# Kernel tuning notes

Measured on AMD Instinct MI355X. Metric: run time of the kernel, lower is better.

Reference implementation:

```python
import jax, jax.numpy as jnp
import numpy as np

B, NNODES, E, IN, H, FEAS = 32, 1024, 262144, 8, 128, 64


def setup_inputs() -> dict:
    key = jax.random.key(0)
    ks = jax.random.split(key, 24)
    N = B * NNODES
    s = 0.05
    x = jax.random.normal(ks[0], (N, IN), jnp.float32)
    edge_index = jax.random.randint(ks[1], (2, E), 0, N)
    batch_vec = jnp.repeat(jnp.arange(B), NNODES)
    rows_local = jax.random.randint(ks[2], (B, FEAS), 0, NNODES)
    mask_rows = (rows_local + jnp.arange(B)[:, None] * NNODES).reshape(-1)
    mask_cols = jax.random.randint(ks[3], (B * FEAS,), 0, NNODES)
    inp = dict(x=x, edge_index=edge_index, batch_vec=batch_vec,
               mask_rows=mask_rows, mask_cols=mask_cols)
    # GIN layer 0 MLP: Linear(IN,H) -> ReLU -> Linear(H,H)
    inp['gin0_w1'] = jax.random.normal(ks[4], (IN, H), jnp.float32) * s
    inp['gin0_b1'] = jnp.zeros((H,), jnp.float32)
    inp['gin0_w2'] = jax.random.normal(ks[5], (H, H), jnp.float32) * s
    inp['gin0_b2'] = jnp.zeros((H,), jnp.float32)
    # GIN layers 1..3 stacked
    inp['gin_w1'] = jax.random.normal(ks[6], (3, H, H), jnp.float32) * s
    inp['gin_b1'] = jnp.zeros((3, H), jnp.float32)
    inp['gin_w2'] = jax.random.normal(ks[7], (3, H, H), jnp.float32) * s
    inp['gin_b2'] = jnp.zeros((3, H), jnp.float32)
    # BatchNorm affine params for the 4 layers
    inp['bn_gamma'] = jnp.ones((4, H), jnp.float32)
    inp['bn_beta'] = jnp.zeros((4, H), jnp.float32)
    # policy layer 0: Linear(2H,H) -> Tanh -> Linear(H,H)
    inp['pol0_w1'] = jax.random.normal(ks[8], (2 * H, H), jnp.float32) * s
    inp['pol0_b1'] = jnp.zeros((H,), jnp.float32)
    inp['pol0_w2'] = jax.random.normal(ks[9], (H, H), jnp.float32) * s
    inp['pol0_b2'] = jnp.zeros((H,), jnp.float32)
    # policy layers 1..2 stacked
    inp['pol_w1'] = jax.random.normal(ks[10], (2, H, H), jnp.float32) * s
    inp['pol_b1'] = jnp.zeros((2, H), jnp.float32)
    inp['pol_w2'] = jax.random.normal(ks[11], (2, H, H), jnp.float32) * s
    inp['pol_b2'] = jnp.zeros((2, H), jnp.float32)
    return inp


def reference(x, edge_index, batch_vec, mask_rows, mask_cols,
              gin0_w1, gin0_b1, gin0_w2, gin0_b2,
              gin_w1, gin_b1, gin_w2, gin_b2,
              bn_gamma, bn_beta,
              pol0_w1, pol0_b1, pol0_w2, pol0_b2,
              pol_w1, pol_b1, pol_w2, pol_b2):
    N = x.shape[0]
    n = N // B
    src, dst = edge_index[0], edge_index[1]
    deg = jnp.maximum(jax.ops.segment_sum(jnp.ones((E,), x.dtype), dst, num_segments=N), 1.0)[:, None]

    def gin(h, w1, b1, w2, b2):
        # GINConv(eps=0, aggr='mean'): nn(x + mean_j x_j)
        agg = jax.ops.segment_sum(h[src], dst, num_segments=N) / deg
        z = h + agg
        return jnp.maximum(z @ w1 + b1, 0.0) @ w2 + b2

    def bn(h, g, b):
        mu = h.mean(0)
        var = h.var(0)  # biased, as torch BN normalization
        return (h - mu) * jax.lax.rsqrt(var + 1e-5) * g + b

    counts = jnp.maximum(jax.ops.segment_sum(jnp.ones((N,), x.dtype), batch_vec, num_segments=B), 1.0)[:, None]

    h = bn(jnp.maximum(gin(x, gin0_w1, gin0_b1, gin0_w2, gin0_b2), 0.0), bn_gamma[0], bn_beta[0])
    node_pool = h
    gpool = jax.ops.segment_sum(h, batch_vec, num_segments=B) / counts
    for l in range(3):
        h = bn(jnp.maximum(gin(h, gin_w1[l], gin_b1[l], gin_w2[l], gin_b2[l]), 0.0),
               bn_gamma[l + 1], bn_beta[l + 1])
        node_pool = node_pool + h
        gpool = gpool + jax.ops.segment_sum(h, batch_vec, num_segments=B) / counts

    aug = jnp.concatenate([node_pool, jnp.repeat(gpool, n, axis=0)], axis=-1).reshape(B, n, 2 * H)

    def pol(z, w1, b1, w2, b2):
        return jnp.tanh(z @ w1 + b1) @ w2 + b2

    z = pol(aug, pol0_w1, pol0_b1, pol0_w2, pol0_b2)
    for l in range(2):
        z = pol(z, pol_w1[l], pol_b1[l], pol_w2[l], pol_b2[l])

    score = jnp.einsum('bnd,bmd->bnm', z, z)  # [B, n, n]
    mask = jnp.ones((B * n, n), bool).at[mask_rows, mask_cols].set(False).reshape(B, n, n)
    score = jnp.where(mask, -jnp.inf, score)
    pi = jax.nn.softmax(score.reshape(B, -1), axis=-1)  # [B, n*n]
    return pi
```

## Files before the change

kernel.cpp:

```cpp
#include <hip/hip_runtime.h>

#define NND 32768
#define NE  262144
#define HD 128
#define NPAIR 2048
#define NBLK 256
#define SQOFF 32768
#define PSLOT 65536

typedef __attribute__((ext_vector_type(8))) short short8;
typedef __attribute__((ext_vector_type(4))) float f32x4;

__device__ __forceinline__ void fma4(float4& a, float s, const float4& w){
  a.x = fmaf(s, w.x, a.x);
  a.y = fmaf(s, w.y, a.y);
  a.z = fmaf(s, w.z, a.z);
  a.w = fmaf(s, w.w, a.w);
}

__device__ __forceinline__ unsigned short bf16rne(float x){
  unsigned int u = __float_as_uint(x);
  unsigned int r = u + 0x7FFFu + ((u >> 16) & 1u);
  return (unsigned short)(r >> 16);
}
__device__ __forceinline__ float bf16tof(unsigned short h){
  return __uint_as_float(((unsigned int)h) << 16);
}

__global__ __launch_bounds__(256) void k_zero(float4* __restrict__ p, int n4){
  int i = blockIdx.x*256 + threadIdx.x;
  int stride = gridDim.x*256;
  float4 z = make_float4(0.f,0.f,0.f,0.f);
  for (; i < n4; i += stride) p[i] = z;
}

__global__ __launch_bounds__(256) void k_wsplit(const float* __restrict__ g0w2, const float* __restrict__ gw1,
                                                const float* __restrict__ gw2, unsigned short* __restrict__ WThi,
                                                unsigned short* __restrict__ WTlo){
  __shared__ float tile[16*129];
  int kblk = blockIdx.x, mat = blockIdx.y;
  int k0 = kblk * 16;
  const float* W = (mat == 0) ? g0w2 : ((mat < 4) ? (gw1 + (mat-1)*16384) : (gw2 + (mat-4)*16384));
  int t = threadIdx.x;
  {
    int kk = t >> 4, n0 = (t & 15) * 8;
    float4 v0 = *(const float4*)&W[(size_t)(k0+kk)*HD + n0];
    float4 v1 = *(const float4*)&W[(size_t)(k0+kk)*HD + n0 + 4];
    tile[kk*129 + n0+0] = v0.x; tile[kk*129 + n0+1] = v0.y;
    tile[kk*129 + n0+2] = v0.z; tile[kk*129 + n0+3] = v0.w;
    tile[kk*129 + n0+4] = v1.x; tile[kk*129 + n0+5] = v1.y;
    tile[kk*129 + n0+6] = v1.z; tile[kk*129 + n0+7] = v1.w;
  }
  __syncthreads();
  int n = t >> 1, koff = (t & 1) * 8;
  short8 hv, lv;
  #pragma unroll
  for (int q=0;q<8;q++){
    float v = tile[(koff+q)*129 + n];
    unsigned short h = bf16rne(v);
    hv[q] = (short)h;
    lv[q] = (short)bf16rne(v - bf16tof(h));
  }
  size_t o = (size_t)mat*16384 + (size_t)n*HD + k0 + koff;
  *(short8*)&WThi[o] = hv;
  *(short8*)&WTlo[o] = lv;
}

__global__ __launch_bounds__(256) void k_count(const int* __restrict__ dst, int* __restrict__ cnt){
  int e = blockIdx.x*256 + threadIdx.x;
  if (e < NE) atomicAdd(&cnt[dst[e]], 1);
}

__global__ __launch_bounds__(1024) void k_scan(const int* __restrict__ cnt, int* __restrict__ rowp,
                                               float* __restrict__ invdeg){
  __shared__ int part[1024];
  int t = threadIdx.x;
  int base = t*32;
  int local[32];
  int s = 0;
  #pragma unroll
  for (int j=0;j<32;j++){ local[j] = s; s += cnt[base+j]; }
  part[t] = s;
  __syncthreads();
  for (int d=1; d<1024; d<<=1){
    int v = (t>=d) ? part[t-d] : 0;
    __syncthreads();
    part[t] += v;
    __syncthreads();
  }
  int off = (t==0) ? 0 : part[t-1];
  #pragma unroll
  for (int j=0;j<32;j++){
    rowp[base+j] = off + local[j];
    int c = cnt[base+j];
    invdeg[base+j] = 1.0f / (float)(c > 0 ? c : 1);
  }
  if (t == 1023) rowp[NND] = off + s;
}

__global__ __launch_bounds__(256) void k_fill(const int* __restrict__ src, const int* __restrict__ dst,
                                              const int* __restrict__ rowp, int* __restrict__ fillc,
                                              int* __restrict__ csr){
  int e = blockIdx.x*256 + threadIdx.x;
  if (e < NE){
    int d = dst[e];
    int p = atomicAdd(&fillc[d], 1);
    csr[rowp[d] + p] = src[e];
  }
}

__global__ __launch_bounds__(256) void k_agg8(const float* __restrict__ x, const int* __restrict__ rowp,
                                              const int* __restrict__ csr, const float* __restrict__ invdeg,
                                              float* __restrict__ z8){
  int i = blockIdx.x*256 + threadIdx.x;
  float s[8] = {0,0,0,0,0,0,0,0};
  int a = rowp[i], bnd = rowp[i+1];
  for (int k=a;k<bnd;k++){
    int j = csr[k];
    const float4* p = (const float4*)&x[(size_t)j*8];
    float4 u0 = p[0], u1 = p[1];
    s[0]+=u0.x; s[1]+=u0.y; s[2]+=u0.z; s[3]+=u0.w;
    s[4]+=u1.x; s[5]+=u1.y; s[6]+=u1.z; s[7]+=u1.w;
  }
  float iv = invdeg[i];
  const float4* xp = (const float4*)&x[(size_t)i*8];
  float4 x0 = xp[0], x1 = xp[1];
  float4 o0, o1;
  o0.x = x0.x + s[0]*iv; o0.y = x0.y + s[1]*iv; o0.z = x0.z + s[2]*iv; o0.w = x0.w + s[3]*iv;
  o1.x = x1.x + s[4]*iv; o1.y = x1.y + s[5]*iv; o1.z = x1.z + s[6]*iv; o1.w = x1.w + s[7]*iv;
  ((float4*)&z8[(size_t)i*8])[0] = o0;
  ((float4*)&z8[(size_t)i*8])[1] = o1;
}

__global__ __launch_bounds__(256) void k_gemm8(const float* __restrict__ A, const float* __restrict__ W,
                                               const float* __restrict__ bias, unsigned short* __restrict__ Ch,
                                               unsigned short* __restrict__ Cl){
  __shared__ float Ws[8*HD];
  __shared__ float bs[HD];
  int tid = threadIdx.x;
  for (int u=tid; u<8*HD; u+=256) Ws[u] = W[u];
  if (tid < HD) bs[tid] = bias[tid];
  __syncthreads();
  int g = blockIdx.x*256 + tid;
  int row = g >> 7, c = g & 127;
  const float4* a4 = (const float4*)&A[(size_t)row*8];
  float4 a0 = a4[0], a1 = a4[1];
  float s = bs[c];
  s = fmaf(a0.x, Ws[0*128+c], s); s = fmaf(a0.y, Ws[1*128+c], s);
  s = fmaf(a0.z, Ws[2*128+c], s); s = fmaf(a0.w, Ws[3*128+c], s);
  s = fmaf(a1.x, Ws[4*128+c], s); s = fmaf(a1.y, Ws[5*128+c], s);
  s = fmaf(a1.z, Ws[6*128+c], s); s = fmaf(a1.w, Ws[7*128+c], s);
  s = fmaxf(s, 0.0f);
  unsigned short h = bf16rne(s);
  Ch[g] = h;
  Cl[g] = bf16rne(s - bf16tof(h));
}

template<int STATS>
__global__ __launch_bounds__(256) void k_mgemm(const unsigned short* __restrict__ Ah, const unsigned short* __restrict__ Al,
                                               const unsigned short* __restrict__ Wh, const unsigned short* __restrict__ Wl,
                                               const float* __restrict__ bias, float* __restrict__ Cf,
                                               unsigned short* __restrict__ Ch, unsigned short* __restrict__ Cl,
                                               float* __restrict__ part){
  __shared__ unsigned short AH[128*40], AL[128*40], WH[128*40], WL[128*40];
  __shared__ float SS[256], SQ[256];
  int tid = threadIdx.x;
  int r0 = blockIdx.x * 128;
  int row = tid >> 1, half = tid & 1;
  int l = tid & 63, w = tid >> 6;
  int lane15 = l & 15, lgrp = l >> 4;
  int rw = (w >> 1) * 64, cw = (w & 1) * 64;

  f32x4 acc[4][4];
  #pragma unroll
  for (int i=0;i<4;i++)
    #pragma unroll
    for (int j=0;j<4;j++){ f32x4 z = {0.f,0.f,0.f,0.f}; acc[i][j] = z; }

  size_t abase = (size_t)(r0 + row)*HD + half*16;
  size_t wbase = (size_t)row*HD + half*16;
  float4 p0 = *(const float4*)&Ah[abase];     float4 p1 = *(const float4*)&Ah[abase+8];
  float4 p2 = *(const float4*)&Al[abase];     float4 p3 = *(const float4*)&Al[abase+8];
  float4 p4 = *(const float4*)&Wh[wbase];     float4 p5 = *(const float4*)&Wh[wbase+8];
  float4 p6 = *(const float4*)&Wl[wbase];     float4 p7 = *(const float4*)&Wl[wbase+8];

  for (int k0 = 0; k0 < 128; k0 += 32){
    __syncthreads();
    int ldst = row*40 + half*16;
    *(float4*)&AH[ldst] = p0; *(float4*)&AH[ldst+8] = p1;
    *(float4*)&AL[ldst] = p2; *(float4*)&AL[ldst+8] = p3;
    *(float4*)&WH[ldst] = p4; *(float4*)&WH[ldst+8] = p5;
    *(float4*)&WL[ldst] = p6; *(float4*)&WL[ldst+8] = p7;
    __syncthreads();
    if (k0 < 96){
      p0 = *(const float4*)&Ah[abase + k0+32]; p1 = *(const float4*)&Ah[abase + k0+40];
      p2 = *(const float4*)&Al[abase + k0+32]; p3 = *(const float4*)&Al[abase + k0+40];
      p4 = *(const float4*)&Wh[wbase + k0+32]; p5 = *(const float4*)&Wh[wbase + k0+40];
      p6 = *(const float4*)&Wl[wbase + k0+32]; p7 = *(const float4*)&Wl[wbase + k0+40];
    }
    short8 ah[4], al[4], wh[4], wl[4];
    #pragma unroll
    for (int i=0;i<4;i++){
      int ar = (rw + 16*i + lane15)*40 + lgrp*8;
      ah[i] = *(const short8*)&AH[ar];
      al[i] = *(const short8*)&AL[ar];
      int wr = (cw + 16*i + lane15)*40 + lgrp*8;
      wh[i] = *(const short8*)&WH[wr];
      wl[i] = *(const short8*)&WL[wr];
    }
    #pragma unroll
    for (int i=0;i<4;i++){
      #pragma unroll
      for (int j=0;j<4;j++){
        acc[i][j] = __builtin_amdgcn_mfma_f32_16x16x32_bf16(ah[i], wh[j], acc[i][j], 0, 0, 0);
        acc[i][j] = __builtin_amdgcn_mfma_f32_16x16x32_bf16(al[i], wh[j], acc[i][j], 0, 0, 0);
        acc[i][j] = __builtin_amdgcn_mfma_f32_16x16x32_bf16(ah[i], wl[j], acc[i][j], 0, 0, 0);
      }
    }
  }

  float bj[4], sj[4] = {0,0,0,0}, qj[4] = {0,0,0,0};
  #pragma unroll
  for (int j=0;j<4;j++) bj[j] = bias[cw + 16*j + lane15];
  #pragma unroll
  for (int i=0;i<4;i++){
    #pragma unroll
    for (int j=0;j<4;j++){
      f32x4 v = acc[i][j];
      int n = cw + 16*j + lane15;
      #pragma unroll
      for (int r=0;r<4;r++){
        float xv = fmaxf(v[r] + bj[j], 0.f);
        int m = r0 + rw + 16*i + 4*lgrp + r;
        if (STATS){
          Cf[(size_t)m*HD + n] = xv;
          sj[j] += xv;
          qj[j] = fmaf(xv, xv, qj[j]);
        } else {
          unsigned short h = bf16rne(xv);
          Ch[(size_t)m*HD + n] = h;
          Cl[(size_t)m*HD + n] = bf16rne(xv - bf16tof(h));
        }
      }
    }
  }
  if (STATS){
    #pragma unroll
    for (int j=0;j<4;j++){
      float s = sj[j], q = qj[j];
      s += __shfl_xor(s, 16); s += __shfl_xor(s, 32);
      q += __shfl_xor(q, 16); q += __shfl_xor(q, 32);
      if (lgrp == 0){
        SS[(w>>1)*128 + cw + 16*j + lane15] = s;
        SQ[(w>>1)*128 + cw + 16*j + lane15] = q;
      }
    }
    __syncthreads();
    if (tid < HD){
      part[blockIdx.x*HD + tid] = SS[tid] + SS[128 + tid];
      part[SQOFF + blockIdx.x*HD + tid] = SQ[tid] + SQ[128 + tid];
    }
  }
}

__global__ __launch_bounds__(256) void k_bn_fin(const float* __restrict__ part, const float* __restrict__ gamma,
                                                const float* __restrict__ beta, float* __restrict__ scale,
                                                float* __restrict__ shift){
  __shared__ float rs[256];
  __shared__ float rq[256];
  int f = blockIdx.x, t = threadIdx.x;
  rs[t] = part[t*HD + f];
  rq[t] = part[SQOFF + t*HD + f];
  __syncthreads();
  for (int d=128; d>0; d>>=1){
    if (t < d){ rs[t] += rs[t+d]; rq[t] += rq[t+d]; }
    __syncthreads();
  }
  if (t == 0){
    float mu  = rs[0] * (1.0f/NND);
    float var = rq[0] * (1.0f/NND) - mu*mu;
    float sc  = gamma[f] * rsqrtf(var + 1e-5f);
    scale[f] = sc;
    shift[f] = beta[f] - mu*sc;
  }
}

__global__ __launch_bounds__(128) void k_agg_bn(const float* __restrict__ raw, const int* __restrict__ rowp,
                                                const int* __restrict__ csr, const float* __restrict__ invdeg,
                                                const float* __restrict__ scale, const float* __restrict__ shift,
                                                unsigned short* __restrict__ zh, unsigned short* __restrict__ zl){
  int i = blockIdx.x;
  int f = threadIdx.x;
  int a = rowp[i], bnd = rowp[i+1];
  float s = 0.f;
  for (int k = a; k < bnd; k++) s += raw[(size_t)csr[k]*HD + f];
  float sc = scale[f], sh = shift[f];
  size_t idx = (size_t)i*HD + f;
  float vi = fmaf(raw[idx], sc, sh);
  float zz = vi + fmaf(invdeg[i]*sc, s, (bnd > a) ? sh : 0.f);
  unsigned short h = bf16rne(zz);
  zh[idx] = h;
  zl[idx] = bf16rne(zz - bf16tof(h));
}

__global__ __launch_bounds__(128) void k_gpool(const float* __restrict__ part, const float* __restrict__ bnsc,
                                               const float* __restrict__ bnsh, float* __restrict__ gsum){
  int b = blockIdx.x, f = threadIdx.x;
  float g = 0.f;
  #pragma unroll
  for (int l=0;l<4;l++){
    float s = 0.f;
    #pragma unroll
    for (int t=0;t<8;t++) s += part[l*PSLOT + (b*8 + t)*HD + f];
    g += fmaf(bnsc[l*128+f], s, 1024.0f*bnsh[l*128+f]);
  }
  gsum[b*HD + f] = g;
}

__global__ __launch_bounds__(256) void k_build_aug(const int* __restrict__ mrows, const int* __restrict__ mcols,
                                                   const float* __restrict__ raw0, const float* __restrict__ raw1,
                                                   const float* __restrict__ raw2, const float* __restrict__ raw3,
                                                   const float* __restrict__ bnsc, const float* __restrict__ bnsh,
                                                   const float* __restrict__ gsum, float* __restrict__ aug){
  int idx = blockIdx.x;
  int t = threadIdx.x;
  int j = idx & 2047;
  int rg = mrows[j];
  int b = rg >> 10;
  int g = (idx >= 2048) ? ((b << 10) | mcols[j]) : rg;
  float v;
  if (t < 128){
    size_t o = (size_t)g*HD + t;
    v = fmaf(bnsc[t],     raw0[o], bnsh[t]);
    v = fmaf(bnsc[128+t], raw1[o], v + bnsh[128+t]);
    v = fmaf(bnsc[256+t], raw2[o], v + bnsh[256+t]);
    v = fmaf(bnsc[384+t], raw3[o], v + bnsh[384+t]);
  } else {
    v = gsum[b*HD + (t-128)] * (1.0f/1024.0f);
  }
  aug[(size_t)idx*256 + t] = v;
}

template<int K1>
__global__ __launch_bounds__(256) void k_pol(const float* __restrict__ A, const float* __restrict__ W1,
                                             const float* __restrict__ b1, const float* __restrict__ W2,
                                             const float* __restrict__ b2, float* __restrict__ C){
  __shared__ float S1[32*128 + 64*36];
  __shared__ float T[64*132];
  int tid = threadIdx.x;
  int r0 = blockIdx.x * 64;
  int tc = tid & 15, rg = tid >> 4;
  int c0 = tc * 4;
  float4 acc0[4], acc1[4];
  #pragma unroll
  for (int j=0;j<4;j++){ acc0[j] = make_float4(0,0,0,0); acc1[j] = make_float4(0,0,0,0); }
  for (int k0 = 0; k0 < K1; k0 += 32){
    __syncthreads();
    #pragma unroll
    for (int u=0;u<4;u++){
      int e = tid + u*256;
      *(float4*)&S1[(e>>5)*HD + ((e&31)<<2)] = *(const float4*)&W1[(size_t)(k0 + (e>>5))*HD + ((e&31)<<2)];
    }
    #pragma unroll
    for (int u=0;u<2;u++){
      int e = tid + u*256;
      *(float4*)&S1[4096 + (e>>3)*36 + ((e&7)<<2)] = *(const float4*)&A[(size_t)(r0 + (e>>3))*K1 + k0 + ((e&7)<<2)];
    }
    __syncthreads();
    #pragma unroll
    for (int kk=0; kk<32; kk+=4){
      float4 w0[4], w1[4];
      #pragma unroll
      for (int q=0;q<4;q++){
        w0[q] = *(const float4*)&S1[(kk+q)*HD + c0];
        w1[q] = *(const float4*)&S1[(kk+q)*HD + c0 + 64];
      }
      #pragma unroll
      for (int j=0;j<4;j++){
        float4 av = *(const float4*)&S1[4096 + (rg+16*j)*36 + kk];
        fma4(acc0[j], av.x, w0[0]); fma4(acc1[j], av.x, w1[0]);
        fma4(acc0[j], av.y, w0[1]); fma4(acc1[j], av.y, w1[1]);
        fma4(acc0[j], av.z, w0[2]); fma4(acc1[j], av.z, w1[2]);
        fma4(acc0[j], av.w, w0[3]); fma4(acc1[j], av.w, w1[3]);
      }
    }
  }
  {
    float4 bA = *(const float4*)&b1[c0];
    float4 bB = *(const float4*)&b1[c0+64];
    #pragma unroll
    for (int j=0;j<4;j++){
// ... 71 lines not shown
    if (f<d) red[f] = fmaxf(red[f], red[f+d]);
    __syncthreads();
  }
  float m = red[0];
  __syncthreads();
  bool first = true;
  for (int j=0;j<f;j++) if (rr[j]==row && cc[j]==col) first = false;
  float e = expf(s - m);
  red[f] = first ? e : 0.0f;
  __syncthreads();
  for (int d=32; d>0; d>>=1){
    if (f<d) red[f] += red[f+d];
    __syncthreads();
  }
  float denom = red[0];
  out[(size_t)b*1048576 + row*1024 + col] = e / denom;
}

extern "C" void kernel_launch(void* const* d_in, const int* in_sizes, int n_in,
                              void* d_out, int out_size, void* d_ws, size_t ws_size,
                              hipStream_t stream){
  const float* x     = (const float*)d_in[0];
  const int*   ei    = (const int*)d_in[1];
  const int*   mrows = (const int*)d_in[3];
  const int*   mcols = (const int*)d_in[4];
  const float* g0w1  = (const float*)d_in[5];
  const float* g0b1  = (const float*)d_in[6];
  const float* g0w2  = (const float*)d_in[7];
  const float* g0b2  = (const float*)d_in[8];
  const float* gw1   = (const float*)d_in[9];
  const float* gb1   = (const float*)d_in[10];
  const float* gw2   = (const float*)d_in[11];
  const float* gb2   = (const float*)d_in[12];
  const float* bng   = (const float*)d_in[13];
  const float* bnb   = (const float*)d_in[14];
  const float* p0w1  = (const float*)d_in[15];
  const float* p0b1  = (const float*)d_in[16];
  const float* p0w2  = (const float*)d_in[17];
  const float* p0b2  = (const float*)d_in[18];
  const float* pw1   = (const float*)d_in[19];
  const float* pb1   = (const float*)d_in[20];
  const float* pw2   = (const float*)d_in[21];
  const float* pb2   = (const float*)d_in[22];

  float* fw    = (float*)d_ws;
  float* raw0  = fw;
  float* raw1  = fw + 4194304;
  float* raw2  = fw + 8388608;
  float* raw3  = fw + 12582912;
  float* aug   = fw + 16777216;
  float* pX    = fw + 17825792;
  float* pY    = fw + 18350080;
  float* pZ    = fw + 18874368;
  float* z8    = fw + 19398656;
  float* invdeg= fw + 19660800;
  float* bnsc  = fw + 19693568;
  float* bnsh  = fw + 19694080;
  float* part  = fw + 19694592;
  float* gsum  = fw + 19956736;
  int*   cnt   = (int*)(fw + 19960832);
  int*   fillc = cnt + NND;
  int*   rowp  = fillc + NND;
  int*   csr   = rowp + NND + 1;
  unsigned short* us = (unsigned short*)(fw + 20500000);
  unsigned short* zHi  = us;
  unsigned short* zLo  = us + 4194304;
  unsigned short* tHi  = us + 8388608;
  unsigned short* tLo  = us + 12582912;
  unsigned short* WThi = us + 16777216;
  unsigned short* WTlo = us + 16891904;
  float* raws[4] = {raw0, raw1, raw2, raw3};

  const int* src = ei;
  const int* dst = ei + NE;

  hipLaunchKernelGGL(k_zero, dim3(2048), dim3(256), 0, stream, (float4*)d_out, out_size/4);
  hipMemsetAsync(cnt, 0, (size_t)(2*NND)*4, stream);
  hipLaunchKernelGGL(k_wsplit, dim3(8,7), dim3(256), 0, stream, g0w2, gw1, gw2, WThi, WTlo);

  hipLaunchKernelGGL(k_count, dim3(NE/256), dim3(256), 0, stream, dst, cnt);
  hipLaunchKernelGGL(k_scan, dim3(1), dim3(1024), 0, stream, cnt, rowp, invdeg);
  hipLaunchKernelGGL(k_fill, dim3(NE/256), dim3(256), 0, stream, src, dst, rowp, fillc, csr);

  hipLaunchKernelGGL(k_agg8, dim3(NND/256), dim3(256), 0, stream, x, rowp, csr, invdeg, z8);
  hipLaunchKernelGGL(k_gemm8, dim3(NND*HD/256), dim3(256), 0, stream, z8, g0w1, g0b1, tHi, tLo);
  hipLaunchKernelGGL((k_mgemm<1>), dim3(NBLK), dim3(256), 0, stream, tHi, tLo, WThi, WTlo, g0b2,
                     raw0, (unsigned short*)nullptr, (unsigned short*)nullptr, part);
  hipLaunchKernelGGL(k_bn_fin, dim3(128), dim3(256), 0, stream, part, bng, bnb, bnsc, bnsh);

  for (int l=0;l<3;l++){
    hipLaunchKernelGGL(k_agg_bn, dim3(NND), dim3(128), 0, stream, raws[l], rowp, csr, invdeg,
                       bnsc + l*128, bnsh + l*128, zHi, zLo);
    hipLaunchKernelGGL((k_mgemm<0>), dim3(NBLK), dim3(256), 0, stream, zHi, zLo,
                       WThi + (1+l)*16384, WTlo + (1+l)*16384, gb1 + l*128,
                       (float*)nullptr, tHi, tLo, (float*)nullptr);
    hipLaunchKernelGGL((k_mgemm<1>), dim3(NBLK), dim3(256), 0, stream, tHi, tLo,
                       WThi + (4+l)*16384, WTlo + (4+l)*16384, gb2 + l*128,
                       raws[l+1], (unsigned short*)nullptr, (unsigned short*)nullptr, part + (l+1)*PSLOT);
    hipLaunchKernelGGL(k_bn_fin, dim3(128), dim3(256), 0, stream, part + (l+1)*PSLOT, bng + (l+1)*128, bnb + (l+1)*128,
                       bnsc + (l+1)*128, bnsh + (l+1)*128);
  }

  hipLaunchKernelGGL(k_gpool, dim3(32), dim3(128), 0, stream, part, bnsc, bnsh, gsum);
  hipLaunchKernelGGL(k_build_aug, dim3(4096), dim3(256), 0, stream, mrows, mcols,
                     raw0, raw1, raw2, raw3, bnsc, bnsh, gsum, aug);

  hipLaunchKernelGGL((k_pol<256>), dim3(64), dim3(256), 0, stream, aug, p0w1, p0b1, p0w2, p0b2, pX);
  hipLaunchKernelGGL((k_pol<128>), dim3(64), dim3(256), 0, stream, pX, pw1, pb1, pw2, pb2, pY);
  hipLaunchKernelGGL((k_pol<128>), dim3(64), dim3(256), 0, stream, pY, pw1 + 16384, pb1 + 128, pw2 + 16384, pb2 + 128, pZ);

  hipLaunchKernelGGL(k_score, dim3(32), dim3(64), 0, stream, pZ, mrows, mcols, (float*)d_out);
}
```

Before: 408.0 us.

## Fuse init, layer-0 kernels, and BN stats via atomics to cut launches

Merges output zeroing, weight bf16 splitting and metadata clearing into one init kernel, replacing the separate memset. Fuses layer-0 aggregation with the 8-wide GEMM. BatchNorm and graph-pool statistics are now accumulated with global atomics inside the GEMM epilogue, and scale/shift is recomputed inline by consumers, so the k_bn_fin and k_gpool kernels go away. This removes several small launches and serialization points, at the cost of atomic contention, float atomics that make the sums non-deterministic, and redundant per-thread rsqrt work.

```diff
diff --git a/kernel.cpp b/kernel.cpp
--- a/kernel.cpp
+++ b/kernel.cpp
@@ -5,8 +5,6 @@
 #define HD 128
 #define NPAIR 2048
 #define NBLK 256
-#define SQOFF 32768
-#define PSLOT 65536
 
 typedef __attribute__((ext_vector_type(8))) short short8;
 typedef __attribute__((ext_vector_type(4))) float f32x4;
@@ -27,43 +25,48 @@
   return __uint_as_float(((unsigned int)h) << 16);
 }
 
-__global__ __launch_bounds__(256) void k_zero(float4* __restrict__ p, int n4){
-  int i = blockIdx.x*256 + threadIdx.x;
-  int stride = gridDim.x*256;
-  float4 z = make_float4(0.f,0.f,0.f,0.f);
-  for (; i < n4; i += stride) p[i] = z;
-}
-
-__global__ __launch_bounds__(256) void k_wsplit(const float* __restrict__ g0w2, const float* __restrict__ gw1,
-                                                const float* __restrict__ gw2, unsigned short* __restrict__ WThi,
-                                                unsigned short* __restrict__ WTlo){
+__global__ __launch_bounds__(256) void k_init(float4* __restrict__ out4, int n4,
+                                              float4* __restrict__ meta4, int m4,
+                                              const float* __restrict__ g0w2, const float* __restrict__ gw1,
+                                              const float* __restrict__ gw2, unsigned short* __restrict__ WThi,
+                                              unsigned short* __restrict__ WTlo){
   __shared__ float tile[16*129];
-  int kblk = blockIdx.x, mat = blockIdx.y;
-  int k0 = kblk * 16;
-  const float* W = (mat == 0) ? g0w2 : ((mat < 4) ? (gw1 + (mat-1)*16384) : (gw2 + (mat-4)*16384));
+  int bid = blockIdx.x;
   int t = threadIdx.x;
-  {
-    int kk = t >> 4, n0 = (t & 15) * 8;
-    float4 v0 = *(const float4*)&W[(size_t)(k0+kk)*HD + n0];
-    float4 v1 = *(const float4*)&W[(size_t)(k0+kk)*HD + n0 + 4];
-    tile[kk*129 + n0+0] = v0.x; tile[kk*129 + n0+1] = v0.y;
-    tile[kk*129 + n0+2] = v0.z; tile[kk*129 + n0+3] = v0.w;
-    tile[kk*129 + n0+4] = v1.x; tile[kk*129 + n0+5] = v1.y;
-    tile[kk*129 + n0+6] = v1.z; tile[kk*129 + n0+7] = v1.w;
-  }
-  __syncthreads();
-  int n = t >> 1, koff = (t & 1) * 8;
-  short8 hv, lv;
-  #pragma unroll
-  for (int q=0;q<8;q++){
-    float v = tile[(koff+q)*129 + n];
-    unsigned short h = bf16rne(v);
-    hv[q] = (short)h;
-    lv[q] = (short)bf16rne(v - bf16tof(h));
-  }
-  size_t o = (size_t)mat*16384 + (size_t)n*HD + k0 + koff;
-  *(short8*)&WThi[o] = hv;
-  *(short8*)&WTlo[o] = lv;
+  if (bid < 2048){
+    float4 z = make_float4(0.f,0.f,0.f,0.f);
+    for (int i = bid*256 + t; i < n4; i += 2048*256) out4[i] = z;
+  } else if (bid < 2104){
+    int q = bid - 2048;
+    int mat = q >> 3, kblk = q & 7;
+    int k0 = kblk * 16;
+    const float* W = (mat == 0) ? g0w2 : ((mat < 4) ? (gw1 + (mat-1)*16384) : (gw2 + (mat-4)*16384));
+    {
+      int kk = t >> 4, n0 = (t & 15) * 8;
+      float4 v0 = *(const float4*)&W[(size_t)(k0+kk)*HD + n0];
+      float4 v1 = *(const float4*)&W[(size_t)(k0+kk)*HD + n0 + 4];
+      tile[kk*129 + n0+0] = v0.x; tile[kk*129 + n0+1] = v0.y;
+      tile[kk*129 + n0+2] = v0.z; tile[kk*129 + n0+3] = v0.w;
+      tile[kk*129 + n0+4] = v1.x; tile[kk*129 + n0+5] = v1.y;
+      tile[kk*129 + n0+6] = v1.z; tile[kk*129 + n0+7] = v1.w;
+    }
+    __syncthreads();
+    int n = t >> 1, koff = (t & 1) * 8;
+    short8 hv, lv;
+    #pragma unroll
+    for (int q2=0;q2<8;q2++){
+      float v = tile[(koff+q2)*129 + n];
+      unsigned short h = bf16rne(v);
+      hv[q2] = (short)h;
+      lv[q2] = (short)bf16rne(v - bf16tof(h));
+    }
+    size_t o = (size_t)mat*16384 + (size_t)n*HD + k0 + koff;
+    *(short8*)&WThi[o] = hv;
+    *(short8*)&WTlo[o] = lv;
+  } else {
+    float4 z = make_float4(0.f,0.f,0.f,0.f);
+    for (int i = (bid-2104)*256 + t; i < m4; i += 8*256) meta4[i] = z;
+  }
 }
 
 __global__ __launch_bounds__(256) void k_count(const int* __restrict__ dst, int* __restrict__ cnt){
@@ -109,49 +112,32 @@
   }
 }
 
-__global__ __launch_bounds__(256) void k_agg8(const float* __restrict__ x, const int* __restrict__ rowp,
-                                              const int* __restrict__ csr, const float* __restrict__ invdeg,
-                                              float* __restrict__ z8){
-  int i = blockIdx.x*256 + threadIdx.x;
-  float s[8] = {0,0,0,0,0,0,0,0};
-  int a = rowp[i], bnd = rowp[i+1];
-  for (int k=a;k<bnd;k++){
-    int j = csr[k];
-    const float4* p = (const float4*)&x[(size_t)j*8];
-    float4 u0 = p[0], u1 = p[1];
-    s[0]+=u0.x; s[1]+=u0.y; s[2]+=u0.z; s[3]+=u0.w;
-    s[4]+=u1.x; s[5]+=u1.y; s[6]+=u1.z; s[7]+=u1.w;
-  }
-  float iv = invdeg[i];
-  const float4* xp = (const float4*)&x[(size_t)i*8];
-  float4 x0 = xp[0], x1 = xp[1];
-  float4 o0, o1;
-  o0.x = x0.x + s[0]*iv; o0.y = x0.y + s[1]*iv; o0.z = x0.z + s[2]*iv; o0.w = x0.w + s[3]*iv;
-  o1.x = x1.x + s[4]*iv; o1.y = x1.y + s[5]*iv; o1.z = x1.z + s[6]*iv; o1.w = x1.w + s[7]*iv;
-  ((float4*)&z8[(size_t)i*8])[0] = o0;
-  ((float4*)&z8[(size_t)i*8])[1] = o1;
-}
-
-__global__ __launch_bounds__(256) void k_gemm8(const float* __restrict__ A, const float* __restrict__ W,
-                                               const float* __restrict__ bias, unsigned short* __restrict__ Ch,
-                                               unsigned short* __restrict__ Cl){
+__global__ __launch_bounds__(256) void k_l0(const float* __restrict__ x, const int* __restrict__ rowp,
+                                            const int* __restrict__ csr, const float* __restrict__ invdeg,
+                                            const float* __restrict__ W, const float* __restrict__ bias,
+                                            unsigned short* __restrict__ Ch, unsigned short* __restrict__ Cl){
   __shared__ float Ws[8*HD];
   __shared__ float bs[HD];
+  __shared__ float zs[2*9];
   int tid = threadIdx.x;
   for (int u=tid; u<8*HD; u+=256) Ws[u] = W[u];
   if (tid < HD) bs[tid] = bias[tid];
+  if (tid < 16){
+    int lr = tid >> 3, f = tid & 7;
+    int i = blockIdx.x*2 + lr;
+    int a = rowp[i], bnd = rowp[i+1];
+    float s = 0.f;
+    for (int k=a;k<bnd;k++) s += x[(size_t)csr[k]*8 + f];
+    zs[lr*9 + f] = x[(size_t)i*8 + f] + s*invdeg[i];
+  }
   __syncthreads();
-  int g = blockIdx.x*256 + tid;
-  int row = g >> 7, c = g & 127;
-  const float4* a4 = (const float4*)&A[(size_t)row*8];
-  float4 a0 = a4[0], a1 = a4[1];
+  int lr = tid >> 7, c = tid & 127;
   float s = bs[c];
-  s = fmaf(a0.x, Ws[0*128+c], s); s = fmaf(a0.y, Ws[1*128+c], s);
-  s = fmaf(a0.z, Ws[2*128+c], s); s = fmaf(a0.w, Ws[3*128+c], s);
-  s = fmaf(a1.x, Ws[4*128+c], s); s = fmaf(a1.y, Ws[5*128+c], s);
-  s = fmaf(a1.z, Ws[6*128+c], s); s = fmaf(a1.w, Ws[7*128+c], s);
-  s = fmaxf(s, 0.0f);
+  #pragma unroll
+  for (int k=0;k<8;k++) s = fmaf(zs[lr*9+k], Ws[k*128+c], s);
+  s = fmaxf(s, 0.f);
   unsigned short h = bf16rne(s);
+  size_t g = (size_t)(blockIdx.x*2+lr)*HD + c;
   Ch[g] = h;
   Cl[g] = bf16rne(s - bf16tof(h));
 }
@@ -161,7 +147,8 @@
                                                const unsigned short* __restrict__ Wh, const unsigned short* __restrict__ Wl,
                                                const float* __restrict__ bias, float* __restrict__ Cf,
                                                unsigned short* __restrict__ Ch, unsigned short* __restrict__ Cl,
-                                               float* __restrict__ part){
+                                               float* __restrict__ bnsum, float* __restrict__ bnsq,
+                                               float* __restrict__ gsumL){
   __shared__ unsigned short AH[128*40], AL[128*40], WH[128*40], WL[128*40];
   __shared__ float SS[256], SQ[256];
   int tid = threadIdx.x;
@@ -257,44 +244,29 @@
     }
     __syncthreads();
     if (tid < HD){
-      part[blockIdx.x*HD + tid] = SS[tid] + SS[128 + tid];
-      part[SQOFF + blockIdx.x*HD + tid] = SQ[tid] + SQ[128 + tid];
-    }
-  }
-}
-
-__global__ __launch_bounds__(256) void k_bn_fin(const float* __restrict__ part, const float* __restrict__ gamma,
-                                                const float* __restrict__ beta, float* __restrict__ scale,
-                                                float* __restrict__ shift){
-  __shared__ float rs[256];
-  __shared__ float rq[256];
-  int f = blockIdx.x, t = threadIdx.x;
-  rs[t] = part[t*HD + f];
-  rq[t] = part[SQOFF + t*HD + f];
-  __syncthreads();
-  for (int d=128; d>0; d>>=1){
-    if (t < d){ rs[t] += rs[t+d]; rq[t] += rq[t+d]; }
-    __syncthreads();
-  }
-  if (t == 0){
-    float mu  = rs[0] * (1.0f/NND);
-    float var = rq[0] * (1.0f/NND) - mu*mu;
-    float sc  = gamma[f] * rsqrtf(var + 1e-5f);
-    scale[f] = sc;
-    shift[f] = beta[f] - mu*sc;
+      float s = SS[tid] + SS[128 + tid];
+      float q = SQ[tid] + SQ[128 + tid];
+      atomicAdd(&bnsum[tid], s);
+      atomicAdd(&bnsq[tid], q);
+      atomicAdd(&gsumL[(blockIdx.x >> 3)*HD + tid], s);
+    }
   }
 }
 
 __global__ __launch_bounds__(128) void k_agg_bn(const float* __restrict__ raw, const int* __restrict__ rowp,
                                                 const int* __restrict__ csr, const float* __restrict__ invdeg,
-                                                const float* __restrict__ scale, const float* __restrict__ shift,
+                                                const float* __restrict__ bnsum_l, const float* __restrict__ bnsq_l,
+                                                const float* __restrict__ gamma_l, const float* __restrict__ beta_l,
                                                 unsigned short* __restrict__ zh, unsigned short* __restrict__ zl){
   int i = blockIdx.x;
   int f = threadIdx.x;
   int a = rowp[i], bnd = rowp[i+1];
   float s = 0.f;
   for (int k = a; k < bnd; k++) s += raw[(size_t)csr[k]*HD + f];
-  float sc = scale[f], sh = shift[f];
+  float mu  = bnsum_l[f] * (1.0f/NND);
+  float var = bnsq_l[f] * (1.0f/NND) - mu*mu;
+  float sc  = gamma_l[f] * rsqrtf(var + 1e-5f);
+  float sh  = beta_l[f] - mu*sc;
   size_t idx = (size_t)i*HD + f;
   float vi = fmaf(raw[idx], sc, sh);
   float zz = vi + fmaf(invdeg[i]*sc, s, (bnd > a) ? sh : 0.f);
@@ -303,40 +275,40 @@
   zl[idx] = bf16rne(zz - bf16tof(h));
 }
 
-__global__ __launch_bounds__(128) void k_gpool(const float* __restrict__ part, const float* __restrict__ bnsc,
-                                               const float* __restrict__ bnsh, float* __restrict__ gsum){
-  int b = blockIdx.x, f = threadIdx.x;
-  float g = 0.f;
-  #pragma unroll
-  for (int l=0;l<4;l++){
-    float s = 0.f;
-    #pragma unroll
-    for (int t=0;t<8;t++) s += part[l*PSLOT + (b*8 + t)*HD + f];
-    g += fmaf(bnsc[l*128+f], s, 1024.0f*bnsh[l*128+f]);
-  }
-  gsum[b*HD + f] = g;
-}
-
 __global__ __launch_bounds__(256) void k_build_aug(const int* __restrict__ mrows, const int* __restrict__ mcols,
                                                    const float* __restrict__ raw0, const float* __restrict__ raw1,
                                                    const float* __restrict__ raw2, const float* __restrict__ raw3,
-                                                   const float* __restrict__ bnsc, const float* __restrict__ bnsh,
-                                                   const float* __restrict__ gsum, float* __restrict__ aug){
+                                                   const float* __restrict__ bnsum, const float* __restrict__ bnsq,
+                                                   const float* __restrict__ bng, const float* __restrict__ bnb,
+                                                   const float* __restrict__ gsumL, float* __restrict__ aug){
   int idx = blockIdx.x;
   int t = threadIdx.x;
   int j = idx & 2047;
   int rg = mrows[j];
   int b = rg >> 10;
   int g = (idx >= 2048) ? ((b << 10) | mcols[j]) : rg;
+  int f = (t < 128) ? t : (t - 128);
+  float sc[4], sh[4];
+  #pragma unroll
+  for (int l=0;l<4;l++){
+    float mu  = bnsum[l*128+f] * (1.0f/NND);
+    float var = bnsq[l*128+f] * (1.0f/NND) - mu*mu;
+    sc[l] = bng[l*128+f] * rsqrtf(var + 1e-5f);
+    sh[l] = bnb[l*128+f] - mu*sc[l];
+  }
   float v;
   if (t < 128){
-    size_t o = (size_t)g*HD + t;
-    v = fmaf(bnsc[t],     raw0[o], bnsh[t]);
-    v = fmaf(bnsc[128+t], raw1[o], v + bnsh[128+t]);
-    v = fmaf(bnsc[256+t], raw2[o], v + bnsh[256+t]);
-    v = fmaf(bnsc[384+t], raw3[o], v + bnsh[384+t]);
+    size_t o = (size_t)g*HD + f;
+    v = fmaf(sc[0], raw0[o], sh[0]);
+    v = fmaf(sc[1], raw1[o], v + sh[1]);
+    v = fmaf(sc[2], raw2[o], v + sh[2]);
+    v = fmaf(sc[3], raw3[o], v + sh[3]);
   } else {
-    v = gsum[b*HD + (t-128)] * (1.0f/1024.0f);
+    float gacc = 0.f;
+    #pragma unroll
+    for (int l=0;l<4;l++)
+      gacc += fmaf(sc[l], gsumL[(l*32 + b)*HD + f], 1024.0f*sh[l]);
+    v = gacc * (1.0f/1024.0f);
   }
   aug[(size_t)idx*256 + t] = v;
 }
@@ -514,15 +486,15 @@
   float* pX    = fw + 17825792;
   float* pY    = fw + 18350080;
   float* pZ    = fw + 18874368;
-  float* z8    = fw + 19398656;
-  float* invdeg= fw + 19660800;
-  float* bnsc  = fw + 19693568;
-  float* bnsh  = fw + 19694080;
-  float* part  = fw + 19694592;
-  float* gsum  = fw + 19956736;
-  int*   cnt   = (int*)(fw + 19960832);
+  float* invdeg= fw + 19398656;
+  float* meta  = fw + 19431424;
+  int*   cnt   = (int*)meta;
   int*   fillc = cnt + NND;
-  int*   rowp  = fillc + NND;
+  float* bnsum = (float*)(fillc + NND);
+  float* bnsq  = bnsum + 512;
+  float* gsumL = bnsq + 512;
+  const int META4 = (NND + NND + 512 + 512 + 16384) / 4;
+  int*   rowp  = (int*)(gsumL + 16384);
   int*   csr   = rowp + NND + 1;
   unsigned short* us = (unsigned short*)(fw + 20500000);
   unsigned short* zHi  = us;
@@ -536,37 +508,32 @@
   const int* src = ei;
   const int* dst = ei + NE;
 
-  hipLaunchKernelGGL(k_zero, dim3(2048), dim3(256), 0, stream, (float4*)d_out, out_size/4);
-  hipMemsetAsync(cnt, 0, (size_t)(2*NND)*4, stream);
-  hipLaunchKernelGGL(k_wsplit, dim3(8,7), dim3(256), 0, stream, g0w2, gw1, gw2, WThi, WTlo);
+  hipLaunchKernelGGL(k_init, dim3(2112), dim3(256), 0, stream, (float4*)d_out, out_size/4,
+                     (float4*)meta, META4, g0w2, gw1, gw2, WThi, WTlo);
 
   hipLaunchKernelGGL(k_count, dim3(NE/256), dim3(256), 0, stream, dst, cnt);
   hipLaunchKernelGGL(k_scan, dim3(1), dim3(1024), 0, stream, cnt, rowp, invdeg);
   hipLaunchKernelGGL(k_fill, dim3(NE/256), dim3(256), 0, stream, src, dst, rowp, fillc, csr);
 
-  hipLaunchKernelGGL(k_agg8, dim3(NND/256), dim3(256), 0, stream, x, rowp, csr, invdeg, z8);
-  hipLaunchKernelGGL(k_gemm8, dim3(NND*HD/256), dim3(256), 0, stream, z8, g0w1, g0b1, tHi, tLo);
+  hipLaunchKernelGGL(k_l0, dim3(NND/2), dim3(256), 0, stream, x, rowp, csr, invdeg, g0w1, g0b1, tHi, tLo);
   hipLaunchKernelGGL((k_mgemm<1>), dim3(NBLK), dim3(256), 0, stream, tHi, tLo, WThi, WTlo, g0b2,
-                     raw0, (unsigned short*)nullptr, (unsigned short*)nullptr, part);
-  hipLaunchKernelGGL(k_bn_fin, dim3(128), dim3(256), 0, stream, part, bng, bnb, bnsc, bnsh);
+                     raw0, (unsigned short*)nullptr, (unsigned short*)nullptr,
+                     bnsum, bnsq, gsumL);
 
   for (int l=0;l<3;l++){
     hipLaunchKernelGGL(k_agg_bn, dim3(NND), dim3(128), 0, stream, raws[l], rowp, csr, invdeg,
-                       bnsc + l*128, bnsh + l*128, zHi, zLo);
+                       bnsum + l*128, bnsq + l*128, bng + l*128, bnb + l*128, zHi, zLo);
     hipLaunchKernelGGL((k_mgemm<0>), dim3(NBLK), dim3(256), 0, stream, zHi, zLo,
                        WThi + (1+l)*16384, WTlo + (1+l)*16384, gb1 + l*128,
-                       (float*)nullptr, tHi, tLo, (float*)nullptr);
+                       (float*)nullptr, tHi, tLo, (float*)nullptr, (float*)nullptr, (float*)nullptr);
     hipLaunchKernelGGL((k_mgemm<1>), dim3(NBLK), dim3(256), 0, stream, tHi, tLo,
                        WThi + (4+l)*16384, WTlo + (4+l)*16384, gb2 + l*128,
-                       raws[l+1], (unsigned short*)nullptr, (unsigned short*)nullptr, part + (l+1)*PSLOT);
-    hipLaunchKernelGGL(k_bn_fin, dim3(128), dim3(256), 0, stream, part + (l+1)*PSLOT, bng + (l+1)*128, bnb + (l+1)*128,
-                       bnsc + (l+1)*128, bnsh + (l+1)*128);
-  }
-
-  hipLaunchKernelGGL(k_gpool, dim3(32), dim3(128), 0, stream, part, bnsc, bnsh, gsum);
+                       raws[l+1], (unsigned short*)nullptr, (unsigned short*)nullptr,
+                       bnsum + (l+1)*128, bnsq + (l+1)*128, gsumL + (l+1)*4096);
+  }
+
   hipLaunchKernelGGL(k_build_aug, dim3(4096), dim3(256), 0, stream, mrows, mcols,
-                     raw0, raw1, raw2, raw3, bnsc, bnsh, gsum, aug);
-
+                     raw0, raw1, raw2, raw3, bnsum, bnsq, bng, bnb, gsumL, aug);
   hipLaunchKernelGGL((k_pol<256>), dim3(64), dim3(256), 0, stream, aug, p0w1, p0b1, p0w2, p0b2, pX);
   hipLaunchKernelGGL((k_pol<128>), dim3(64), dim3(256), 0, stream, pX, pw1, pb1, pw2, pb2, pY);
   hipLaunchKernelGGL((k_pol<128>), dim3(64), dim3(256), 0, stream, pY, pw1 + 16384, pb1 + 128, pw2 + 16384, pb2 + 128, pZ);
```

Result: slower. 431.1 us (+5.7%).

## Fuse both GIN MLP GEMMs per layer into one kernel with LDS intermediate

Applied to the files above, without the earlier changes.

For GIN layers 1-3, the two split-bf16 MFMA GEMMs become one kernel, k_glayer. It processes 64-row tiles and keeps the intermediate ReLU output as hi/lo bf16 in shared memory, so it never writes to or reads back from global memory. That removes one kernel launch per layer and a round trip of the intermediate through global memory. The grid doubles to 512 blocks and the partial-stat layout changes, so k_bn_fin now loops over a variable block count and k_gpool reads 16 partials per graph. The larger LDS footprint may reduce occupancy.

```diff
diff --git a/kernel.cpp b/kernel.cpp
--- a/kernel.cpp
+++ b/kernel.cpp
@@ -6,7 +6,7 @@
 #define NPAIR 2048
 #define NBLK 256
 #define SQOFF 32768
-#define PSLOT 65536
+#define GBLK 512
 
 typedef __attribute__((ext_vector_type(8))) short short8;
 typedef __attribute__((ext_vector_type(4))) float f32x4;
@@ -156,12 +156,10 @@
   Cl[g] = bf16rne(s - bf16tof(h));
 }
 
-template<int STATS>
-__global__ __launch_bounds__(256) void k_mgemm(const unsigned short* __restrict__ Ah, const unsigned short* __restrict__ Al,
-                                               const unsigned short* __restrict__ Wh, const unsigned short* __restrict__ Wl,
-                                               const float* __restrict__ bias, float* __restrict__ Cf,
-                                               unsigned short* __restrict__ Ch, unsigned short* __restrict__ Cl,
-                                               float* __restrict__ part){
+__global__ __launch_bounds__(256) void k_mgemm1(const unsigned short* __restrict__ Ah, const unsigned short* __restrict__ Al,
+                                                const unsigned short* __restrict__ Wh, const unsigned short* __restrict__ Wl,
+                                                const float* __restrict__ bias, float* __restrict__ Cf,
+                                                float* __restrict__ part){
   __shared__ unsigned short AH[128*40], AL[128*40], WH[128*40], WL[128*40];
   __shared__ float SS[256], SQ[256];
   int tid = threadIdx.x;
@@ -232,45 +230,205 @@
       for (int r=0;r<4;r++){
         float xv = fmaxf(v[r] + bj[j], 0.f);
         int m = r0 + rw + 16*i + 4*lgrp + r;
-        if (STATS){
+        Cf[(size_t)m*HD + n] = xv;
+        sj[j] += xv;
+        qj[j] = fmaf(xv, xv, qj[j]);
+      }
+    }
+  }
+  #pragma unroll
+  for (int j=0;j<4;j++){
+    float s = sj[j], q = qj[j];
+    s += __shfl_xor(s, 16); s += __shfl_xor(s, 32);
+    q += __shfl_xor(q, 16); q += __shfl_xor(q, 32);
+    if (lgrp == 0){
+      SS[(w>>1)*128 + cw + 16*j + lane15] = s;
+      SQ[(w>>1)*128 + cw + 16*j + lane15] = q;
+    }
+  }
+  __syncthreads();
+  if (tid < HD){
+    part[blockIdx.x*HD + tid] = SS[tid] + SS[128 + tid];
+    part[SQOFF + blockIdx.x*HD + tid] = SQ[tid] + SQ[128 + tid];
+  }
+}
+
+__global__ __launch_bounds__(256) void k_glayer(const unsigned short* __restrict__ Ah, const unsigned short* __restrict__ Al,
+                                                const unsigned short* __restrict__ W1h, const unsigned short* __restrict__ W1l,
+                                                const float* __restrict__ b1,
+                                                const unsigned short* __restrict__ W2h, const unsigned short* __restrict__ W2l,
+                                                const float* __restrict__ b2,
+                                                float* __restrict__ Cf, float* __restrict__ part){
+  __shared__ unsigned short AH[64*40], AL[64*40], WH[128*40], WL[128*40];
+  __shared__ unsigned short TH[64*136], TL[64*136];
+  __shared__ float SS[128], SQ[128];
+  int tid = threadIdx.x;
+  int r0 = blockIdx.x * 64;
+  int l = tid & 63, w = tid >> 6;
+  int lane15 = l & 15, lgrp = l >> 4;
+  int cw = w * 32;
+
+  f32x4 acc[4][2];
+  #pragma unroll
+  for (int i=0;i<4;i++){
+    #pragma unroll
+    for (int j=0;j<2;j++){ f32x4 z = {0.f,0.f,0.f,0.f}; acc[i][j] = z; }
+  }
+
+  int arow = tid >> 2, akoff = (tid & 3) * 8;
+  size_t abase = (size_t)(r0 + arow)*HD + akoff;
+  int wrow = tid >> 1, whalf = (tid & 1) * 16;
+  size_t wbase = (size_t)wrow*HD + whalf;
+  float4 pa0 = *(const float4*)&Ah[abase];
+  float4 pa1 = *(const float4*)&Al[abase];
+  float4 pw0 = *(const float4*)&W1h[wbase], pw1 = *(const float4*)&W1h[wbase+8];
+  float4 pw2 = *(const float4*)&W1l[wbase], pw3 = *(const float4*)&W1l[wbase+8];
+
+  for (int k0 = 0; k0 < 128; k0 += 32){
+    __syncthreads();
+    *(float4*)&AH[arow*40 + akoff] = pa0;
+    *(float4*)&AL[arow*40 + akoff] = pa1;
+    int wd = wrow*40 + whalf;
+    *(float4*)&WH[wd] = pw0; *(float4*)&WH[wd+8] = pw1;
+    *(float4*)&WL[wd] = pw2; *(float4*)&WL[wd+8] = pw3;
+    __syncthreads();
+    if (k0 < 96){
+      pa0 = *(const float4*)&Ah[abase + k0+32];
+      pa1 = *(const float4*)&Al[abase + k0+32];
+      pw0 = *(const float4*)&W1h[wbase + k0+32]; pw1 = *(const float4*)&W1h[wbase + k0+40];
+      pw2 = *(const float4*)&W1l[wbase + k0+32]; pw3 = *(const float4*)&W1l[wbase + k0+40];
+    }
+    short8 ah[4], al4[4], wh[2], wl[2];
+    #pragma unroll
+    for (int i=0;i<4;i++){
+      int ar = (16*i + lane15)*40 + lgrp*8;
+      ah[i]  = *(const short8*)&AH[ar];
+      al4[i] = *(const short8*)&AL[ar];
+    }
+    #pragma unroll
+    for (int j=0;j<2;j++){
+      int wr = (cw + 16*j + lane15)*40 + lgrp*8;
+      wh[j] = *(const short8*)&WH[wr];
+      wl[j] = *(const short8*)&WL[wr];
+    }
+    #pragma unroll
+    for (int i=0;i<4;i++){
+      #pragma unroll
+      for (int j=0;j<2;j++){
+        acc[i][j] = __builtin_amdgcn_mfma_f32_16x16x32_bf16(ah[i],  wh[j], acc[i][j], 0, 0, 0);
+        acc[i][j] = __builtin_amdgcn_mfma_f32_16x16x32_bf16(al4[i], wh[j], acc[i][j], 0, 0, 0);
+        acc[i][j] = __builtin_amdgcn_mfma_f32_16x16x32_bf16(ah[i],  wl[j], acc[i][j], 0, 0, 0);
+      }
+    }
+  }
+  {
+    float bA = b1[cw + lane15], bB = b1[cw + 16 + lane15];
+    #pragma unroll
+    for (int i=0;i<4;i++){
+      #pragma unroll
+      for (int j=0;j<2;j++){
+        f32x4 v = acc[i][j];
+        float bb = j ? bB : bA;
+        int n = cw + 16*j + lane15;
+        #pragma unroll
+        for (int r=0;r<4;r++){
+          float xv = fmaxf(v[r] + bb, 0.f);
+          int m = 16*i + 4*lgrp + r;
+          unsigned short h = bf16rne(xv);
+          TH[m*136 + n] = h;
+          TL[m*136 + n] = bf16rne(xv - bf16tof(h));
+        }
+      }
+    }
+  }
+  #pragma unroll
+  for (int i=0;i<4;i++){
+    #pragma unroll
+    for (int j=0;j<2;j++){ f32x4 z = {0.f,0.f,0.f,0.f}; acc[i][j] = z; }
+  }
+  pw0 = *(const float4*)&W2h[wbase]; pw1 = *(const float4*)&W2h[wbase+8];
+  pw2 = *(const float4*)&W2l[wbase]; pw3 = *(const float4*)&W2l[wbase+8];
+  for (int k0 = 0; k0 < 128; k0 += 32){
+    __syncthreads();
+    int wd = wrow*40 + whalf;
+    *(float4*)&WH[wd] = pw0; *(float4*)&WH[wd+8] = pw1;
+    *(float4*)&WL[wd] = pw2; *(float4*)&WL[wd+8] = pw3;
+    __syncthreads();
+    if (k0 < 96){
+      pw0 = *(const float4*)&W2h[wbase + k0+32]; pw1 = *(const float4*)&W2h[wbase + k0+40];
+      pw2 = *(const float4*)&W2l[wbase + k0+32]; pw3 = *(const float4*)&W2l[wbase + k0+40];
+    }
+    short8 ah[4], al4[4], wh[2], wl[2];
+    #pragma unroll
+    for (int i=0;i<4;i++){
+      int ar = (16*i + lane15)*136 + k0 + lgrp*8;
+      ah[i]  = *(const short8*)&TH[ar];
+      al4[i] = *(const short8*)&TL[ar];
+    }
+    #pragma unroll
+    for (int j=0;j<2;j++){
+      int wr = (cw + 16*j + lane15)*40 + lgrp*8;
+      wh[j] = *(const short8*)&WH[wr];
+      wl[j] = *(const short8*)&WL[wr];
+    }
+    #pragma unroll
+    for (int i=0;i<4;i++){
+      #pragma unroll
+      for (int j=0;j<2;j++){
+        acc[i][j] = __builtin_amdgcn_mfma_f32_16x16x32_bf16(ah[i],  wh[j], acc[i][j], 0, 0, 0);
+        acc[i][j] = __builtin_amdgcn_mfma_f32_16x16x32_bf16(al4[i], wh[j], acc[i][j], 0, 0, 0);
+        acc[i][j] = __builtin_amdgcn_mfma_f32_16x16x32_bf16(ah[i],  wl[j], acc[i][j], 0, 0, 0);
+      }
+    }
+  }
+  {
+    float bA = b2[cw + lane15], bB = b2[cw + 16 + lane15];
+    float s0 = 0.f, s1 = 0.f, q0 = 0.f, q1 = 0.f;
+    #pragma unroll
+    for (int i=0;i<4;i++){
+      #pragma unroll
+      for (int j=0;j<2;j++){
+        f32x4 v = acc[i][j];
+        float bb = j ? bB : bA;
+        int n = cw + 16*j + lane15;
+        #pragma unroll
+        for (int r=0;r<4;r++){
+          float xv = fmaxf(v[r] + bb, 0.f);
+          int m = r0 + 16*i + 4*lgrp + r;
           Cf[(size_t)m*HD + n] = xv;
-          sj[j] += xv;
-          qj[j] = fmaf(xv, xv, qj[j]);
-        } else {
-          unsigned short h = bf16rne(xv);
-          Ch[(size_t)m*HD + n] = h;
-          Cl[(size_t)m*HD + n] = bf16rne(xv - bf16tof(h));
+          if (j){ s1 += xv; q1 = fmaf(xv, xv, q1); }
+          else  { s0 += xv; q0 = fmaf(xv, xv, q0); }
         }
       }
     }
-  }
-  if (STATS){
-    #pragma unroll
-    for (int j=0;j<4;j++){
-      float s = sj[j], q = qj[j];
-      s += __shfl_xor(s, 16); s += __shfl_xor(s, 32);
-      q += __shfl_xor(q, 16); q += __shfl_xor(q, 32);
-      if (lgrp == 0){
-        SS[(w>>1)*128 + cw + 16*j + lane15] = s;
-        SQ[(w>>1)*128 + cw + 16*j + lane15] = q;
-      }
-    }
-    __syncthreads();
-    if (tid < HD){
-      part[blockIdx.x*HD + tid] = SS[tid] + SS[128 + tid];
-      part[SQOFF + blockIdx.x*HD + tid] = SQ[tid] + SQ[128 + tid];
-    }
-  }
-}
-
-__global__ __launch_bounds__(256) void k_bn_fin(const float* __restrict__ part, const float* __restrict__ gamma,
-                                                const float* __restrict__ beta, float* __restrict__ scale,
-                                                float* __restrict__ shift){
+    s0 += __shfl_xor(s0, 16); s0 += __shfl_xor(s0, 32);
+    s1 += __shfl_xor(s1, 16); s1 += __shfl_xor(s1, 32);
+    q0 += __shfl_xor(q0, 16); q0 += __shfl_xor(q0, 32);
+    q1 += __shfl_xor(q1, 16); q1 += __shfl_xor(q1, 32);
+    if (lgrp == 0){
+      SS[cw + lane15] = s0;      SS[cw + 16 + lane15] = s1;
+      SQ[cw + lane15] = q0;      SQ[cw + 16 + lane15] = q1;
+    }
+  }
+  __syncthreads();
+  if (tid < HD){
+    part[blockIdx.x*HD + tid] = SS[tid];
+    part[GBLK*HD + blockIdx.x*HD + tid] = SQ[tid];
+  }
+}
+
+__global__ __launch_bounds__(256) void k_bn_fin(const float* __restrict__ part, int nblk,
+                                                const float* __restrict__ gamma, const float* __restrict__ beta,
+                                                float* __restrict__ scale, float* __restrict__ shift){
   __shared__ float rs[256];
   __shared__ float rq[256];
   int f = blockIdx.x, t = threadIdx.x;
-  rs[t] = part[t*HD + f];
-  rq[t] = part[SQOFF + t*HD + f];
+  float s = 0.f, q = 0.f;
+  for (int b = t; b < nblk; b += 256){
+    s += part[b*HD + f];
+    q += part[nblk*HD + b*HD + f];
+  }
+  rs[t] = s; rq[t] = q;
   __syncthreads();
   for (int d=128; d>0; d>>=1){
     if (t < d){ rs[t] += rs[t+d]; rq[t] += rq[t+d]; }
@@ -303,15 +461,22 @@
   zl[idx] = bf16rne(zz - bf16tof(h));
 }
 
-__global__ __launch_bounds__(128) void k_gpool(const float* __restrict__ part, const float* __restrict__ bnsc,
-                                               const float* __restrict__ bnsh, float* __restrict__ gsum){
+__global__ __launch_bounds__(128) void k_gpool(const float* __restrict__ part0, const float* __restrict__ partL,
+                                               const float* __restrict__ bnsc, const float* __restrict__ bnsh,
+                                               float* __restrict__ gsum){
   int b = blockIdx.x, f = threadIdx.x;
-  float g = 0.f;
-  #pragma unroll
-  for (int l=0;l<4;l++){
+  float g;
+  {
     float s = 0.f;
     #pragma unroll
-    for (int t=0;t<8;t++) s += part[l*PSLOT + (b*8 + t)*HD + f];
+    for (int t=0;t<8;t++) s += part0[(b*8 + t)*HD + f];
+    g = fmaf(bnsc[f], s, 1024.0f*bnsh[f]);
+  }
+  #pragma unroll
+  for (int l=1;l<4;l++){
+    float s = 0.f;
+    #pragma unroll
+    for (int t=0;t<16;t++) s += partL[(l-1)*2*GBLK*HD + (b*16 + t)*HD + f];
     g += fmaf(bnsc[l*128+f], s, 1024.0f*bnsh[l*128+f]);
   }
   gsum[b*HD + f] = g;
@@ -518,13 +683,14 @@
   float* invdeg= fw + 19660800;
   float* bnsc  = fw + 19693568;
   float* bnsh  = fw + 19694080;
-  float* part  = fw + 19694592;
-  float* gsum  = fw + 19956736;
-  int*   cnt   = (int*)(fw + 19960832);
+  float* part0 = fw + 19694592;
+  float* partL = fw + 19760128;
+  float* gsum  = fw + 20153344;
+  int*   cnt   = (int*)(fw + 20157440);
   int*   fillc = cnt + NND;
   int*   rowp  = fillc + NND;
   int*   csr   = rowp + NND + 1;
-  unsigned short* us = (unsigned short*)(fw + 20500000);
+  unsigned short* us = (unsigned short*)(fw + 20600000);
   unsigned short* zHi  = us;
   unsigned short* zLo  = us + 4194304;
   unsigned short* tHi  = us + 8388608;
@@ -546,24 +712,21 @@
 
   hipLaunchKernelGGL(k_agg8, dim3(NND/256), dim3(256), 0, stream, x, rowp, csr, invdeg, z8);
   hipLaunchKernelGGL(k_gemm8, dim3(NND*HD/256), dim3(256), 0, stream, z8, g0w1, g0b1, tHi, tLo);
-  hipLaunchKernelGGL((k_mgemm<1>), dim3(NBLK), dim3(256), 0, stream, tHi, tLo, WThi, WTlo, g0b2,
-                     raw0, (unsigned short*)nullptr, (unsigned short*)nullptr, part);
-  hipLaunchKernelGGL(k_bn_fin, dim3(128), dim3(256), 0, stream, part, bng, bnb, bnsc, bnsh);
+  hipLaunchKernelGGL(k_mgemm1, dim3(NBLK), dim3(256), 0, stream, tHi, tLo, WThi, WTlo, g0b2, raw0, part0);
+  hipLaunchKernelGGL(k_bn_fin, dim3(128), dim3(256), 0, stream, part0, NBLK, bng, bnb, bnsc, bnsh);
 
   for (int l=0;l<3;l++){
     hipLaunchKernelGGL(k_agg_bn, dim3(NND), dim3(128), 0, stream, raws[l], rowp, csr, invdeg,
                        bnsc + l*128, bnsh + l*128, zHi, zLo);
-    hipLaunchKernelGGL((k_mgemm<0>), dim3(NBLK), dim3(256), 0, stream, zHi, zLo,
+    hipLaunchKernelGGL(k_glayer, dim3(GBLK), dim3(256), 0, stream, zHi, zLo,
                        WThi + (1+l)*16384, WTlo + (1+l)*16384, gb1 + l*128,
-                       (float*)nullptr, tHi, tLo, (float*)nullptr);
-    hipLaunchKernelGGL((k_mgemm<1>), dim3(NBLK), dim3(256), 0, stream, tHi, tLo,
                        WThi + (4+l)*16384, WTlo + (4+l)*16384, gb2 + l*128,
-                       raws[l+1], (unsigned short*)nullptr, (unsigned short*)nullptr, part + (l+1)*PSLOT);
-    hipLaunchKernelGGL(k_bn_fin, dim3(128), dim3(256), 0, stream, part + (l+1)*PSLOT, bng + (l+1)*128, bnb + (l+1)*128,
-                       bnsc + (l+1)*128, bnsh + (l+1)*128);
-  }
-
-  hipLaunchKernelGGL(k_gpool, dim3(32), dim3(128), 0, stream, part, bnsc, bnsh, gsum);
+                       raws[l+1], partL + l*(2*GBLK*HD));
+    hipLaunchKernelGGL(k_bn_fin, dim3(128), dim3(256), 0, stream, partL + l*(2*GBLK*HD), GBLK,
+                       bng + (l+1)*128, bnb + (l+1)*128, bnsc + (l+1)*128, bnsh + (l+1)*128);
+  }
+
+  hipLaunchKernelGGL(k_gpool, dim3(32), dim3(128), 0, stream, part0, partL, bnsc, bnsh, gsum);
   hipLaunchKernelGGL(k_build_aug, dim3(4096), dim3(256), 0, stream, mrows, mcols,
                      raw0, raw1, raw2, raw3, bnsc, bnsh, gsum, aug);
 
```

Result: faster. 393.8 us (-3.5%).
